# Kernel optimization log

Measured on AMD Instinct MI355X. Metric: run time of the kernel, lower is better.

Reference implementation:

```python
import jax, jax.numpy as jnp
import numpy as np

D_IN = 1024
D_OUT = 1024
NUM_HEADS = 16
HEAD_DIM = D_OUT // NUM_HEADS
ORDERS = 4


def setup_inputs() -> dict:
    key = jax.random.key(0)
    k_x, k_t, k_w, k_b, k_a = jax.random.split(key, 5)
    x = jax.random.normal(k_x, (8, 4096, D_IN), dtype=jnp.float32)
    t_scalar = jax.random.uniform(k_t, (), dtype=jnp.float32)
    # Linear params (torch nn.Linear: y = x @ W.T + b)
    W = jax.random.normal(k_w, (D_OUT, D_IN), dtype=jnp.float32) * (1.0 / np.sqrt(D_IN))
    b = jax.random.normal(k_b, (D_OUT,), dtype=jnp.float32) * 0.01
    A = jax.random.normal(k_a, (NUM_HEADS, HEAD_DIM, HEAD_DIM), dtype=jnp.float32) * 0.02
    return {"x": x, "t_scalar": t_scalar, "W": W, "b": b, "A": A}


def reference(x, t_scalar, W, b, A):
    # proj_in
    z = jnp.einsum('bsd,od->bso', x, W) + b  # [B, S, d_out]
    B, S, _ = z.shape
    z = z.reshape(B, S, NUM_HEADS, HEAD_DIM)
    # Taylor series: out = sum_{k=0}^{ORDERS} (t*A)^k z / k!
    out = z
    term = z
    for order in range(1, ORDERS + 1):
        term = jnp.einsum('hij,bnhj->bnhi', A, term) * (t_scalar / float(order))
        out = out + term
    return out.reshape(B, S, D_OUT)
```

## Files before the change

### kernel.cpp

```cpp
#include <hip/hip_runtime.h>
#include <hip/hip_bf16.h>
#include <cstdint>

#define NHEAD 16
#define ORDERS 4

typedef short short8 __attribute__((ext_vector_type(8)));
typedef float f32x4 __attribute__((ext_vector_type(4)));

__device__ __forceinline__ unsigned short f32_to_bf16_rtn(float f) {
  union { float f; unsigned u; } v; v.f = f;
  unsigned r = v.u + 0x7FFFu + ((v.u >> 16) & 1u);
  return (unsigned short)(r >> 16);
}

typedef __attribute__((address_space(1))) void gvoid;
typedef __attribute__((address_space(3))) void svoid;
__device__ __forceinline__ void gload_lds16(const void* g, void* l) {
  __builtin_amdgcn_global_load_lds((gvoid*)g, (svoid*)l, 16, 0, 0);
}

__global__ __launch_bounds__(256) void weff_kernel(
    const float* __restrict__ A, const float* __restrict__ t_ptr,
    const float* __restrict__ W, const float* __restrict__ bvec,
    unsigned short* __restrict__ Weff, float* __restrict__ beff) {
  __shared__ float Ah[64 * 65];
  __shared__ float T0[64 * 64];
  __shared__ float T1[64 * 64];

  const int tid = threadIdx.x;
  const int h = blockIdx.x >> 4;
  const int c = blockIdx.x & 15;
  const int d = tid & 63;
  const int ig = tid >> 6;

  float wreg[16];
  #pragma unroll
  for (int r = 0; r < 16; ++r)
    wreg[r] = W[(size_t)(h * 64 + ig * 16 + r) * 1024 + c * 64 + d];

  const float t = t_ptr[0];
  const int i = tid >> 2;
  const int jq = (tid & 3) << 4;

  for (int r = 0; r < 16; ++r) {
    int idx = tid + 256 * r;
    Ah[(idx >> 6) * 65 + (idx & 63)] = A[h * 4096 + idx];
  }
  float ms[16];
  #pragma unroll
  for (int cc = 0; cc < 16; ++cc) {
    float e = (i == jq + cc) ? 1.0f : 0.0f;
    T0[i * 64 + jq + cc] = e;
    ms[cc] = e;
  }
  __syncthreads();

  float* Tc = T0;
  float* Tn = T1;
  for (int k = 1; k <= ORDERS; ++k) {
    float scale = t / (float)k;
    float acc[16];
    #pragma unroll
    for (int cc = 0; cc < 16; ++cc) acc[cc] = 0.f;
    for (int l = 0; l < 64; ++l) {
      float a = Ah[i * 65 + l];
      float4 t0 = *(const float4*)&Tc[l * 64 + jq];
      float4 t1 = *(const float4*)&Tc[l * 64 + jq + 4];
      float4 t2 = *(const float4*)&Tc[l * 64 + jq + 8];
      float4 t3 = *(const float4*)&Tc[l * 64 + jq + 12];
      acc[0] += a * t0.x;  acc[1] += a * t0.y;  acc[2] += a * t0.z;  acc[3] += a * t0.w;
      acc[4] += a * t1.x;  acc[5] += a * t1.y;  acc[6] += a * t1.z;  acc[7] += a * t1.w;
      acc[8] += a * t2.x;  acc[9] += a * t2.y;  acc[10] += a * t2.z; acc[11] += a * t2.w;
      acc[12] += a * t3.x; acc[13] += a * t3.y; acc[14] += a * t3.z; acc[15] += a * t3.w;
    }
    #pragma unroll
    for (int cc = 0; cc < 16; ++cc) { acc[cc] *= scale; ms[cc] += acc[cc]; }
    #pragma unroll
    for (int u = 0; u < 4; ++u) {
      float4 v = {acc[u * 4], acc[u * 4 + 1], acc[u * 4 + 2], acc[u * 4 + 3]};
      *(float4*)&Tn[i * 64 + jq + u * 4] = v;
    }
    __syncthreads();
    float* tmp = Tc; Tc = Tn; Tn = tmp;
  }

  float* Mh = Ah;
  #pragma unroll
  for (int u = 0; u < 4; ++u) {
    float4 v = {ms[u * 4], ms[u * 4 + 1], ms[u * 4 + 2], ms[u * 4 + 3]};
    *(float4*)&Mh[i * 64 + jq + u * 4] = v;
  }
  float* Wc = T0;
  #pragma unroll
  for (int r = 0; r < 16; ++r) Wc[(ig * 16 + r) * 64 + d] = wreg[r];
  __syncthreads();

  #pragma unroll
  for (int ii = 0; ii < 16; ++ii) {
    int i2 = ig * 16 + ii;
    float acc = 0.f;
    #pragma unroll
    for (int j = 0; j < 64; ++j) acc += Mh[i2 * 64 + j] * Wc[j * 64 + d];
    Weff[(size_t)(h * 64 + i2) * 1024 + c * 64 + d] = f32_to_bf16_rtn(acc);
  }
  if (c == 0 && tid < 64) {
    float acc = 0.f;
    for (int j = 0; j < 64; ++j) acc += Mh[tid * 64 + j] * bvec[h * 64 + j];
    beff[h * 64 + tid] = acc;
  }
}

__global__ __launch_bounds__(256) void convert_x_kernel(
    const float* __restrict__ X, unsigned short* __restrict__ Xb, int n8) {
  int idx = blockIdx.x * blockDim.x + threadIdx.x;
  int stride = gridDim.x * blockDim.x;
  for (int i = idx; i < n8; i += stride) {
    float4 a = *(const float4*)(X + (size_t)i * 8);
    float4 b = *(const float4*)(X + (size_t)i * 8 + 4);
    unsigned short t[8] = {f32_to_bf16_rtn(a.x), f32_to_bf16_rtn(a.y),
                           f32_to_bf16_rtn(a.z), f32_to_bf16_rtn(a.w),
                           f32_to_bf16_rtn(b.x), f32_to_bf16_rtn(b.y),
                           f32_to_bf16_rtn(b.z), f32_to_bf16_rtn(b.w)};
    *(uint4*)(Xb + (size_t)i * 8) = *(const uint4*)t;
  }
}

#define CSTR 132

__global__ __launch_bounds__(256, 2) void gemm_kernel(
    const unsigned short* __restrict__ Xb, const unsigned short* __restrict__ Wf,
    const float* __restrict__ beff, float* __restrict__ Out) {
  __shared__ __align__(16) unsigned short smem[4 * 8192];

  const int wg = blockIdx.x;
  const int swz = (wg & 7) * 256 + (wg >> 3);
  const int by = swz >> 3;
  const int bx = swz & 7;
  const int R = by * 128;
  const int C = bx * 128;

  const int tid = threadIdx.x;
  const int lane = tid & 63;
  const int wave = tid >> 6;
  const int wm = wave >> 1;
  const int wn = wave & 1;
  const int frow = lane & 15;
  const int fkg = lane >> 4;

  f32x4 acc[4][4];
  #pragma unroll
  for (int mi = 0; mi < 4; ++mi)
    #pragma unroll
    for (int ni = 0; ni < 4; ++ni) acc[mi][ni] = (f32x4){0.f, 0.f, 0.f, 0.f};

  const int lr = lane >> 3;
  const int lc = lane & 7;
  const int scol = ((lc ^ lr) << 3);
  const unsigned short* Asrc = Xb + (size_t)(R + wave * 32 + lr) * 1024 + scol;
  const unsigned short* Bsrc = Wf + (size_t)(C + wave * 32 + lr) * 1024 + scol;

  auto stage = [&](int kt) {
    unsigned short* base = smem + (kt & 1) * 16384;
    char* Ad = (char*)(base + wave * 32 * 64);
    char* Bd = (char*)(base + 8192 + wave * 32 * 64);
    const int kb = kt * 64;
    #pragma unroll
    for (int i = 0; i < 4; ++i)
      gload_lds16(Asrc + (size_t)(i * 8) * 1024 + kb, Ad + i * 1024);
    #pragma unroll
    for (int i = 0; i < 4; ++i)
      gload_lds16(Bsrc + (size_t)(i * 8) * 1024 + kb, Bd + i * 1024);
  };

  stage(0);
  for (int kt = 0; kt < 16; ++kt) {
    if (kt < 15) {
      stage(kt + 1);
      asm volatile("s_waitcnt vmcnt(8)" ::: "memory");
    } else {
      asm volatile("s_waitcnt vmcnt(0)" ::: "memory");
    }
    __builtin_amdgcn_sched_barrier(0);
    __builtin_amdgcn_s_barrier();

    const unsigned short* As = smem + (kt & 1) * 16384;
    const unsigned short* Bs = As + 8192;
    short8 afr[4][2], bfr[4][2];
    #pragma unroll
    for (int mi = 0; mi < 4; ++mi) {
      int ar = wm * 64 + mi * 16 + frow;
      #pragma unroll
      for (int kk = 0; kk < 2; ++kk) {
        int slot = (kk * 4 + fkg) ^ (ar & 7);
        afr[mi][kk] = *(const short8*)&As[ar * 64 + slot * 8];
      }
    }
    #pragma unroll
    for (int ni = 0; ni < 4; ++ni) {
      int br = wn * 64 + ni * 16 + frow;
      #pragma unroll
      for (int kk = 0; kk < 2; ++kk) {
        int slot = (kk * 4 + fkg) ^ (br & 7);
        bfr[ni][kk] = *(const short8*)&Bs[br * 64 + slot * 8];
      }
    }
    asm volatile("s_waitcnt lgkmcnt(0)" ::: "memory");
    __builtin_amdgcn_sched_barrier(0);
    __builtin_amdgcn_s_barrier();

    #pragma unroll
    for (int mi = 0; mi < 4; ++mi)
      #pragma unroll
      for (int ni = 0; ni < 4; ++ni)
        #pragma unroll
        for (int kk = 0; kk < 2; ++kk)
          acc[mi][ni] = __builtin_amdgcn_mfma_f32_16x16x32_bf16(
              afr[mi][kk], bfr[ni][kk], acc[mi][ni], 0, 0, 0);
  }
  __syncthreads();

  float* Cs = (float*)smem;
  const int c4 = (tid & 31) << 2;
  float4 bb = *(const float4*)&beff[C + c4];
  #pragma unroll
  for (int mi = 0; mi < 4; ++mi) {
    #pragma unroll
    for (int ni = 0; ni < 4; ++ni) {
      int col = wn * 64 + ni * 16 + frow;
      #pragma unroll
      for (int reg = 0; reg < 4; ++reg)
        Cs[(wm * 16 + fkg * 4 + reg) * CSTR + col] = acc[mi][ni][reg];
    }
    __syncthreads();
    #pragma unroll
    for (int it = 0; it < 4; ++it) {
      int rloc = it * 8 + (tid >> 5);
      float4 v = *(const float4*)&Cs[rloc * CSTR + c4];
      v.x += bb.x; v.y += bb.y; v.z += bb.z; v.w += bb.w;
      int grow = R + (rloc >> 4) * 64 + mi * 16 + (rloc & 15);
      *(float4*)(Out + (size_t)grow * 1024 + C + c4) = v;
    }
    __syncthreads();
  }
}

#define LDSS 72
#define CSTRF 136
__global__ __launch_bounds__(256, 2) void gemm_fb(
    const float* __restrict__ X, const unsigned short* __restrict__ Weff,
    const float* __restrict__ beff, float* __restrict__ Out) {
  __shared__ __align__(16) unsigned short As0[128 * LDSS];
  __shared__ __align__(16) unsigned short As1[128 * LDSS];
  __shared__ __align__(16) unsigned short Bs0[128 * LDSS];
  __shared__ __align__(16) unsigned short Bs1[128 * LDSS];
  const int wg = blockIdx.x;
  const int swz = (wg & 7) * 256 + (wg >> 3);
  const int R = (swz >> 3) * 128;
  const int C = (swz & 7) * 128;
  const int tid = threadIdx.x;
  const int lane = tid & 63;
  const int wave = tid >> 6;
  const int wm = wave >> 1, wn = wave & 1;
  const int frow = lane & 15, fkg = lane >> 4;
  f32x4 acc[4][4];
  #pragma unroll
  for (int mi = 0; mi < 4; ++mi)
    #pragma unroll
    for (int ni = 0; ni < 4; ++ni) acc[mi][ni] = (f32x4){0.f, 0.f, 0.f, 0.f};
  const int ar = tid >> 4, akc = (tid & 15) << 2;
  const int bn_ = tid >> 3, bkc = (tid & 7) << 3;
  const float* Xbase = X + (size_t)(R + ar) * 1024 + akc;
  const unsigned short* Wbase = Weff + (size_t)(C + bn_) * 1024 + bkc;
  float4 av[8];
  uint4 bv[4];
  auto loadTile = [&](int kt) {
    const int kb = kt * 64;
    #pragma unroll
    for (int i = 0; i < 8; ++i) av[i] = *(const float4*)(Xbase + (size_t)i * 16 * 1024 + kb);
    #pragma unroll
    for (int i = 0; i < 4; ++i) bv[i] = *(const uint4*)(Wbase + (size_t)i * 32 * 1024 + kb);
  };
  auto writeTile = [&](unsigned short* Asn, unsigned short* Bsn) {
    #pragma unroll
    for (int i = 0; i < 8; ++i) {
      unsigned short tmp[4] = {f32_to_bf16_rtn(av[i].x), f32_to_bf16_rtn(av[i].y),
                               f32_to_bf16_rtn(av[i].z), f32_to_bf16_rtn(av[i].w)};
      *(uint2*)&Asn[(ar + i * 16) * LDSS + akc] = *(const uint2*)tmp;
    }
    #pragma unroll
    for (int i = 0; i < 4; ++i) *(uint4*)&Bsn[(bn_ + i * 32) * LDSS + bkc] = bv[i];
  };
  loadTile(0);
  writeTile(As0, Bs0);
  __syncthreads();
  unsigned short* Asc = As0; unsigned short* Asn = As1;
  unsigned short* Bsc = Bs0; unsigned short* Bsn = Bs1;
  for (int kt = 0; kt < 16; ++kt) {
    if (kt < 15) loadTile(kt + 1);
    short8 afr[4][2], bfr[4][2];
    #pragma unroll
    for (int mi = 0; mi < 4; ++mi)
      #pragma unroll
      for (int kk = 0; kk < 2; ++kk)
        afr[mi][kk] = *(const short8*)&Asc[(wm * 64 + mi * 16 + frow) * LDSS + kk * 32 + fkg * 8];
    #pragma unroll
    for (int ni = 0; ni < 4; ++ni)
      #pragma unroll
      for (int kk = 0; kk < 2; ++kk)
        bfr[ni][kk] = *(const short8*)&Bsc[(wn * 64 + ni * 16 + frow) * LDSS + kk * 32 + fkg * 8];
    #pragma unroll
    for (int mi = 0; mi < 4; ++mi)
      #pragma unroll
      for (int ni = 0; ni < 4; ++ni)
        #pragma unroll
        for (int kk = 0; kk < 2; ++kk)
          acc[mi][ni] = __builtin_amdgcn_mfma_f32_16x16x32_bf16(
              afr[mi][kk], bfr[ni][kk], acc[mi][ni], 0, 0, 0);
    if (kt < 15) writeTile(Asn, Bsn);
    __syncthreads();
    unsigned short* t1 = Asc; Asc = Asn; Asn = t1;
    unsigned short* t2 = Bsc; Bsc = Bsn; Bsn = t2;
  }
  float* Cs = (float*)As0;
  const int c4 = (tid & 31) << 2;
  float4 bb = *(const float4*)&beff[C + c4];
  #pragma unroll
  for (int mi = 0; mi < 4; ++mi) {
    #pragma unroll
    for (int ni = 0; ni < 4; ++ni) {
      int col = wn * 64 + ni * 16 + frow;
      #pragma unroll
      for (int reg = 0; reg < 4; ++reg)
        Cs[(wm * 16 + fkg * 4 + reg) * CSTRF + col] = acc[mi][ni][reg];
    }
    __syncthreads();
    #pragma unroll
    for (int it = 0; it < 4; ++it) {
      int rloc = it * 8 + (tid >> 5);
      float4 v = *(const float4*)&Cs[rloc * CSTRF + c4];
      v.x += bb.x; v.y += bb.y; v.z += bb.z; v.w += bb.w;
      int grow = R + (rloc >> 4) * 64 + mi * 16 + (rloc & 15);
      *(float4*)(Out + (size_t)grow * 1024 + C + c4) = v;
    }
    __syncthreads();
  }
}

extern "C" void kernel_launch(void* const* d_in, const int* in_sizes, int n_in,
                              void* d_out, int out_size, void* d_ws, size_t ws_size,
                              hipStream_t stream) {
  const float* x = (const float*)d_in[0];
  const float* t = (const float*)d_in[1];
  const float* W = (const float*)d_in[2];
  const float* b = (const float*)d_in[3];
  const float* A = (const float*)d_in[4];
  float* out = (float*)d_out;

  char* ws = (char*)d_ws;
  unsigned short* Weff = (unsigned short*)ws;
  float* beff = (float*)(ws + (2 << 20));
  unsigned short* Xb = (unsigned short*)(ws + (4ull << 20));

  const size_t need = (4ull << 20) + (64ull << 20);
  weff_kernel<<<256, 256, 0, stream>>>(A, t, W, b, Weff, beff);
  if (ws_size >= need) {
    convert_x_kernel<<<2048, 256, 0, stream>>>(x, Xb, 33554432 / 8);
    gemm_kernel<<<2048, 256, 0, stream>>>(Xb, Weff, beff, out);
  } else {
    gemm_fb<<<2048, 256, 0, stream>>>(x, Weff, beff, out);
  }
}
```

Baseline: 148.3 us.

## Switch bf16 GEMM to 256x256 tiles with phased 8-wave MFMA pipeline

Replaces the 128x128, 4-wave GEMM with a 256x256 tile computed by 8 waves, splitting each K step into four phases that interleave LDS fragment reads, async global-to-LDS staging, and MFMA blocks raised with s_setprio. The larger tile raises arithmetic intensity and cuts global and LDS traffic per output. The epilogue is rewritten to stage 64-row slabs through LDS with bias added. It uses 128KB of LDS per block and many more accumulator registers, which limits occupancy and leaves only 512 blocks.

Result: slower. 172.5 us (+16.3%).

```diff
diff --git a/kernel.cpp b/kernel.cpp
--- a/kernel.cpp
+++ b/kernel.cpp
@@ -126,120 +126,171 @@
   }
 }
 
-#define CSTR 132
-
-__global__ __launch_bounds__(256, 2) void gemm_kernel(
+#define MM16(MOFF, BSET, NOFF)                                                 \
+  {                                                                            \
+    _Pragma("unroll") for (int m_ = 0; m_ < 4; ++m_)                           \
+        _Pragma("unroll") for (int n_ = 0; n_ < 2; ++n_)                       \
+            _Pragma("unroll") for (int kk_ = 0; kk_ < 2; ++kk_)                \
+                acc[MOFF + m_][NOFF + n_] =                                    \
+        __builtin_amdgcn_mfma_f32_16x16x32_bf16(                               \
+            afr[m_][kk_], BSET[n_][kk_], acc[MOFF + m_][NOFF + n_], 0, 0, 0);  \
+  }
+
+__global__ __launch_bounds__(512, 2) void gemm256_kernel(
     const unsigned short* __restrict__ Xb, const unsigned short* __restrict__ Wf,
     const float* __restrict__ beff, float* __restrict__ Out) {
-  __shared__ __align__(16) unsigned short smem[4 * 8192];
+  __shared__ __align__(16) unsigned short smem[2 * 32768];
 
   const int wg = blockIdx.x;
-  const int swz = (wg & 7) * 256 + (wg >> 3);
-  const int by = swz >> 3;
-  const int bx = swz & 7;
-  const int R = by * 128;
-  const int C = bx * 128;
+  const int swz = (wg & 7) * 64 + (wg >> 3);
+  const int R = (swz >> 2) * 256;
+  const int C = (swz & 3) * 256;
 
   const int tid = threadIdx.x;
   const int lane = tid & 63;
-  const int wave = tid >> 6;
-  const int wm = wave >> 1;
-  const int wn = wave & 1;
+  const int w = tid >> 6;
+  const int wm = w >> 2;
+  const int wn = w & 3;
   const int frow = lane & 15;
   const int fkg = lane >> 4;
-
-  f32x4 acc[4][4];
-  #pragma unroll
-  for (int mi = 0; mi < 4; ++mi)
+  const int rx = frow & 7;
+
+  const int lr = lane >> 3;
+  const int scol = ((lane & 7) ^ lr) << 3;
+  const unsigned short* AsrcB = Xb + (size_t)(R + w * 8 + lr) * 1024 + scol;
+  const unsigned short* BsrcB = Wf + (size_t)(C + w * 8 + lr) * 1024 + scol;
+
+  auto stageB = [&](int j) {
+    char* bd = (char*)(smem + (j & 1) * 32768 + 16384) + w * 1024;
+    const unsigned short* s = BsrcB + j * 64;
+    #pragma unroll
+    for (int g = 0; g < 4; ++g)
+      gload_lds16(s + (size_t)(g * 64) * 1024, bd + g * 8192);
+  };
+  auto stageA = [&](int j, int half) {
+    char* ad = (char*)(smem + (j & 1) * 32768) + w * 1024;
+    const unsigned short* s = AsrcB + j * 64;
+    #pragma unroll
+    for (int g = 0; g < 2; ++g) {
+      int q = half + 2 * g;
+      gload_lds16(s + (size_t)(q * 64) * 1024, ad + q * 8192);
+    }
+  };
+
+  f32x4 acc[8][4];
+  #pragma unroll
+  for (int mi = 0; mi < 8; ++mi)
     #pragma unroll
     for (int ni = 0; ni < 4; ++ni) acc[mi][ni] = (f32x4){0.f, 0.f, 0.f, 0.f};
 
-  const int lr = lane >> 3;
-  const int lc = lane & 7;
-  const int scol = ((lc ^ lr) << 3);
-  const unsigned short* Asrc = Xb + (size_t)(R + wave * 32 + lr) * 1024 + scol;
-  const unsigned short* Bsrc = Wf + (size_t)(C + wave * 32 + lr) * 1024 + scol;
-
-  auto stage = [&](int kt) {
-    unsigned short* base = smem + (kt & 1) * 16384;
-    char* Ad = (char*)(base + wave * 32 * 64);
-    char* Bd = (char*)(base + 8192 + wave * 32 * 64);
-    const int kb = kt * 64;
-    #pragma unroll
-    for (int i = 0; i < 4; ++i)
-      gload_lds16(Asrc + (size_t)(i * 8) * 1024 + kb, Ad + i * 1024);
-    #pragma unroll
-    for (int i = 0; i < 4; ++i)
-      gload_lds16(Bsrc + (size_t)(i * 8) * 1024 + kb, Bd + i * 1024);
-  };
-
-  stage(0);
-  for (int kt = 0; kt < 16; ++kt) {
-    if (kt < 15) {
-      stage(kt + 1);
-      asm volatile("s_waitcnt vmcnt(8)" ::: "memory");
-    } else {
-      asm volatile("s_waitcnt vmcnt(0)" ::: "memory");
-    }
-    __builtin_amdgcn_sched_barrier(0);
-    __builtin_amdgcn_s_barrier();
-
-    const unsigned short* As = smem + (kt & 1) * 16384;
-    const unsigned short* Bs = As + 8192;
-    short8 afr[4][2], bfr[4][2];
-    #pragma unroll
-    for (int mi = 0; mi < 4; ++mi) {
-      int ar = wm * 64 + mi * 16 + frow;
-      #pragma unroll
-      for (int kk = 0; kk < 2; ++kk) {
-        int slot = (kk * 4 + fkg) ^ (ar & 7);
-        afr[mi][kk] = *(const short8*)&As[ar * 64 + slot * 8];
-      }
-    }
-    #pragma unroll
-    for (int ni = 0; ni < 4; ++ni) {
-      int br = wn * 64 + ni * 16 + frow;
-      #pragma unroll
-      for (int kk = 0; kk < 2; ++kk) {
-        int slot = (kk * 4 + fkg) ^ (br & 7);
-        bfr[ni][kk] = *(const short8*)&Bs[br * 64 + slot * 8];
-      }
-    }
+  short8 afr[4][2], b0[2][2], b1[2][2];
+  const int arow0 = wm * 128 + frow;
+  const int brow0 = wn * 64 + frow;
+  const int slot0 = (fkg ^ rx) << 3;
+  const int slot1 = ((4 + fkg) ^ rx) << 3;
+
+  auto rdA = [&](const unsigned short* buf, int msh) {
+    #pragma unroll
+    for (int m = 0; m < 4; ++m) {
+      int r = (arow0 + (msh * 4 + m) * 16) * 64;
+      afr[m][0] = *(const short8*)&buf[r + slot0];
+      afr[m][1] = *(const short8*)&buf[r + slot1];
+    }
+  };
+  auto rdB = [&](const unsigned short* buf, int nsh, short8 (&dst)[2][2]) {
+    #pragma unroll
+    for (int n = 0; n < 2; ++n) {
+      int r = 16384 + (brow0 + (nsh * 2 + n) * 16) * 64;
+      dst[n][0] = *(const short8*)&buf[r + slot0];
+      dst[n][1] = *(const short8*)&buf[r + slot1];
+    }
+  };
+
+  stageB(0);
+  stageA(0, 0);
+  stageA(0, 1);
+  stageA(1, 0);
+  stageA(1, 1);
+  asm volatile("s_waitcnt vmcnt(4)" ::: "memory");
+  __builtin_amdgcn_sched_barrier(0);
+  __builtin_amdgcn_s_barrier();
+
+  for (int j = 0; j < 16; ++j) {
+    const unsigned short* buf = smem + (j & 1) * 32768;
+
+    rdA(buf, 0);
+    rdB(buf, 0, b0);
+    if (j + 1 < 16) stageB(j + 1);
+    __builtin_amdgcn_s_barrier();
     asm volatile("s_waitcnt lgkmcnt(0)" ::: "memory");
     __builtin_amdgcn_sched_barrier(0);
-    __builtin_amdgcn_s_barrier();
-
-    #pragma unroll
-    for (int mi = 0; mi < 4; ++mi)
+    __builtin_amdgcn_s_setprio(1);
+    MM16(0, b0, 0);
+    __builtin_amdgcn_s_setprio(0);
+    __builtin_amdgcn_s_barrier();
+
+    rdB(buf, 1, b1);
+    if (j + 2 < 16) stageA(j + 2, 0);
+    __builtin_amdgcn_s_barrier();
+    asm volatile("s_waitcnt lgkmcnt(0)" ::: "memory");
+    __builtin_amdgcn_sched_barrier(0);
+    __builtin_amdgcn_s_setprio(1);
+    MM16(0, b1, 2);
+    __builtin_amdgcn_s_setprio(0);
+    __builtin_amdgcn_s_barrier();
+
+    rdA(buf, 1);
+    __builtin_amdgcn_s_barrier();
+    asm volatile("s_waitcnt lgkmcnt(0)" ::: "memory");
+    __builtin_amdgcn_sched_barrier(0);
+    __builtin_amdgcn_s_setprio(1);
+    MM16(4, b1, 2);
+    __builtin_amdgcn_s_setprio(0);
+    __builtin_amdgcn_s_barrier();
+
+    rdB(buf, 0, b0);
+    if (j + 2 < 16) stageA(j + 2, 1);
+    __builtin_amdgcn_s_barrier();
+    asm volatile("s_waitcnt lgkmcnt(0)" ::: "memory");
+    __builtin_amdgcn_sched_barrier(0);
+    __builtin_amdgcn_s_setprio(1);
+    MM16(4, b0, 0);
+    __builtin_amdgcn_s_setprio(0);
+    if (j <= 13) {
+      asm volatile("s_waitcnt vmcnt(4)" ::: "memory");
+    } else if (j == 14) {
+      asm volatile("s_waitcnt vmcnt(0)" ::: "memory");
+    }
+    __builtin_amdgcn_sched_barrier(0);
+    __builtin_amdgcn_s_barrier();
+  }
+  __syncthreads();
+
+  float* Cs = (float*)smem;
+  const int er = tid >> 3;
+  const int ecg = tid & 7;
+  float4 bias[8];
+  #pragma unroll
+  for (int u = 0; u < 8; ++u)
+    bias[u] = *(const float4*)&beff[C + ecg * 32 + u * 4];
+  #pragma unroll
+  for (int c = 0; c < 4; ++c) {
+    if (wm == (c >> 1)) {
       #pragma unroll
-      for (int ni = 0; ni < 4; ++ni)
+      for (int m = 0; m < 4; ++m)
         #pragma unroll
-        for (int kk = 0; kk < 2; ++kk)
-          acc[mi][ni] = __builtin_amdgcn_mfma_f32_16x16x32_bf16(
-              afr[mi][kk], bfr[ni][kk], acc[mi][ni], 0, 0, 0);
-  }
-  __syncthreads();
-
-  float* Cs = (float*)smem;
-  const int c4 = (tid & 31) << 2;
-  float4 bb = *(const float4*)&beff[C + c4];
-  #pragma unroll
-  for (int mi = 0; mi < 4; ++mi) {
-    #pragma unroll
-    for (int ni = 0; ni < 4; ++ni) {
-      int col = wn * 64 + ni * 16 + frow;
-      #pragma unroll
-      for (int reg = 0; reg < 4; ++reg)
-        Cs[(wm * 16 + fkg * 4 + reg) * CSTR + col] = acc[mi][ni][reg];
-    }
-    __syncthreads();
-    #pragma unroll
-    for (int it = 0; it < 4; ++it) {
-      int rloc = it * 8 + (tid >> 5);
-      float4 v = *(const float4*)&Cs[rloc * CSTR + c4];
-      v.x += bb.x; v.y += bb.y; v.z += bb.z; v.w += bb.w;
-      int grow = R + (rloc >> 4) * 64 + mi * 16 + (rloc & 15);
-      *(float4*)(Out + (size_t)grow * 1024 + C + c4) = v;
+        for (int ni = 0; ni < 4; ++ni)
+          #pragma unroll
+          for (int reg = 0; reg < 4; ++reg)
+            Cs[(m * 16 + fkg * 4 + reg) * 260 + wn * 64 + ni * 16 + frow] =
+                acc[(c & 1) * 4 + m][ni][reg];
+    }
+    __syncthreads();
+    #pragma unroll
+    for (int u = 0; u < 8; ++u) {
+      float4 v = *(const float4*)&Cs[er * 260 + ecg * 32 + u * 4];
+      v.x += bias[u].x; v.y += bias[u].y; v.z += bias[u].z; v.w += bias[u].w;
+      *(float4*)(Out + (size_t)(R + c * 64 + er) * 1024 + C + ecg * 32 + u * 4) = v;
     }
     __syncthreads();
   }
@@ -366,7 +417,7 @@
   weff_kernel<<<256, 256, 0, stream>>>(A, t, W, b, Weff, beff);
   if (ws_size >= need) {
     convert_x_kernel<<<2048, 256, 0, stream>>>(x, Xb, 33554432 / 8);
-    gemm_kernel<<<2048, 256, 0, stream>>>(Xb, Weff, beff, out);
+    gemm256_kernel<<<512, 512, 0, stream>>>(Xb, Weff, beff, out);
   } else {
     gemm_fb<<<2048, 256, 0, stream>>>(x, Weff, beff, out);
   }
```

## Enlarge GEMM tile to 256x256 with 8 waves and split LDS-read/MFMA phases

Applied to the files above, without the earlier changes.

Replaces the 128x128, 4-wave GEMM with a 256x256 tile using 512 threads and 128KB of double-buffered LDS. The larger tile halves global traffic per output. The main loop now splits A-fragment reads into two halves so the first MFMA batch can start while the second half of LDS reads is still in flight, and it drops one barrier and adds s_setprio around the MFMA blocks. In exchange, occupancy drops to one workgroup per CU, register pressure rises with 128 accumulator floats per thread, and the epilogue is reorganised into four 64-row store passes.

Result: slower. 175.6 us (+18.4%).

```diff
diff --git a/kernel.cpp b/kernel.cpp
--- a/kernel.cpp
+++ b/kernel.cpp
@@ -126,57 +126,54 @@
   }
 }
 
-#define CSTR 132
-
-__global__ __launch_bounds__(256, 2) void gemm_kernel(
+__global__ __launch_bounds__(512, 1) void gemm256_kernel(
     const unsigned short* __restrict__ Xb, const unsigned short* __restrict__ Wf,
     const float* __restrict__ beff, float* __restrict__ Out) {
-  __shared__ __align__(16) unsigned short smem[4 * 8192];
+  __shared__ __align__(16) char smem[131072];
 
   const int wg = blockIdx.x;
-  const int swz = (wg & 7) * 256 + (wg >> 3);
-  const int by = swz >> 3;
-  const int bx = swz & 7;
-  const int R = by * 128;
-  const int C = bx * 128;
+  const int swz = (wg & 7) * 64 + (wg >> 3);
+  const int R = (swz >> 2) * 256;
+  const int C = (swz & 3) * 256;
 
   const int tid = threadIdx.x;
   const int lane = tid & 63;
-  const int wave = tid >> 6;
-  const int wm = wave >> 1;
-  const int wn = wave & 1;
+  const int w = tid >> 6;
+  const int wm = w >> 2;
+  const int wn = w & 3;
   const int frow = lane & 15;
   const int fkg = lane >> 4;
-
-  f32x4 acc[4][4];
-  #pragma unroll
-  for (int mi = 0; mi < 4; ++mi)
+  const int fx = frow & 7;
+
+  f32x4 acc[8][4];
+  #pragma unroll
+  for (int mi = 0; mi < 8; ++mi)
     #pragma unroll
     for (int ni = 0; ni < 4; ++ni) acc[mi][ni] = (f32x4){0.f, 0.f, 0.f, 0.f};
 
-  const int lr = lane >> 3;
-  const int lc = lane & 7;
-  const int scol = ((lc ^ lr) << 3);
-  const unsigned short* Asrc = Xb + (size_t)(R + wave * 32 + lr) * 1024 + scol;
-  const unsigned short* Bsrc = Wf + (size_t)(C + wave * 32 + lr) * 1024 + scol;
+  const int lr8 = lane >> 3;
+  const int sl = lane & 7;
+  const int scol = ((sl ^ lr8) << 3);
+  const unsigned short* Asrc = Xb + (size_t)(R + w * 32 + lr8) * 1024 + scol;
+  const unsigned short* Bsrc = Wf + (size_t)(C + w * 32 + lr8) * 1024 + scol;
 
   auto stage = [&](int kt) {
-    unsigned short* base = smem + (kt & 1) * 16384;
-    char* Ad = (char*)(base + wave * 32 * 64);
-    char* Bd = (char*)(base + 8192 + wave * 32 * 64);
+    char* base = smem + (kt & 1) * 65536;
+    char* Ad = base + w * 4096;
+    char* Bd = base + 32768 + w * 4096;
     const int kb = kt * 64;
     #pragma unroll
-    for (int i = 0; i < 4; ++i)
-      gload_lds16(Asrc + (size_t)(i * 8) * 1024 + kb, Ad + i * 1024);
-    #pragma unroll
-    for (int i = 0; i < 4; ++i)
-      gload_lds16(Bsrc + (size_t)(i * 8) * 1024 + kb, Bd + i * 1024);
+    for (int u = 0; u < 4; ++u)
+      gload_lds16(Asrc + (size_t)(u * 8) * 1024 + kb, Ad + u * 1024);
+    #pragma unroll
+    for (int u = 0; u < 4; ++u)
+      gload_lds16(Bsrc + (size_t)(u * 8) * 1024 + kb, Bd + u * 1024);
   };
 
   stage(0);
-  for (int kt = 0; kt < 16; ++kt) {
-    if (kt < 15) {
-      stage(kt + 1);
+  for (int j = 0; j < 16; ++j) {
+    if (j < 15) {
+      stage(j + 1);
       asm volatile("s_waitcnt vmcnt(8)" ::: "memory");
     } else {
       asm volatile("s_waitcnt vmcnt(0)" ::: "memory");
@@ -184,31 +181,41 @@
     __builtin_amdgcn_sched_barrier(0);
     __builtin_amdgcn_s_barrier();
 
-    const unsigned short* As = smem + (kt & 1) * 16384;
-    const unsigned short* Bs = As + 8192;
-    short8 afr[4][2], bfr[4][2];
-    #pragma unroll
-    for (int mi = 0; mi < 4; ++mi) {
-      int ar = wm * 64 + mi * 16 + frow;
-      #pragma unroll
-      for (int kk = 0; kk < 2; ++kk) {
-        int slot = (kk * 4 + fkg) ^ (ar & 7);
-        afr[mi][kk] = *(const short8*)&As[ar * 64 + slot * 8];
-      }
-    }
+    const unsigned short* As = (const unsigned short*)(smem + (j & 1) * 65536);
+    const unsigned short* Bs = (const unsigned short*)(smem + (j & 1) * 65536 + 32768);
+
+    short8 bfr[4][2], afr0[4][2], afr1[4][2];
     #pragma unroll
     for (int ni = 0; ni < 4; ++ni) {
       int br = wn * 64 + ni * 16 + frow;
       #pragma unroll
       for (int kk = 0; kk < 2; ++kk) {
-        int slot = (kk * 4 + fkg) ^ (br & 7);
+        int slot = (kk * 4 + fkg) ^ fx;
         bfr[ni][kk] = *(const short8*)&Bs[br * 64 + slot * 8];
       }
     }
-    asm volatile("s_waitcnt lgkmcnt(0)" ::: "memory");
+    #pragma unroll
+    for (int mi = 0; mi < 4; ++mi) {
+      int ar = wm * 128 + mi * 16 + frow;
+      #pragma unroll
+      for (int kk = 0; kk < 2; ++kk) {
+        int slot = (kk * 4 + fkg) ^ fx;
+        afr0[mi][kk] = *(const short8*)&As[ar * 64 + slot * 8];
+      }
+    }
     __builtin_amdgcn_sched_barrier(0);
-    __builtin_amdgcn_s_barrier();
-
+    #pragma unroll
+    for (int mi = 0; mi < 4; ++mi) {
+      int ar = wm * 128 + 64 + mi * 16 + frow;
+      #pragma unroll
+      for (int kk = 0; kk < 2; ++kk) {
+        int slot = (kk * 4 + fkg) ^ fx;
+        afr1[mi][kk] = *(const short8*)&As[ar * 64 + slot * 8];
+      }
+    }
+    asm volatile("s_waitcnt lgkmcnt(8)" ::: "memory");
+    __builtin_amdgcn_sched_barrier(0);
+    __builtin_amdgcn_s_setprio(1);
     #pragma unroll
     for (int mi = 0; mi < 4; ++mi)
       #pragma unroll
@@ -216,30 +223,49 @@
         #pragma unroll
         for (int kk = 0; kk < 2; ++kk)
           acc[mi][ni] = __builtin_amdgcn_mfma_f32_16x16x32_bf16(
-              afr[mi][kk], bfr[ni][kk], acc[mi][ni], 0, 0, 0);
+              afr0[mi][kk], bfr[ni][kk], acc[mi][ni], 0, 0, 0);
+    __builtin_amdgcn_s_setprio(0);
+    asm volatile("s_waitcnt lgkmcnt(0)" ::: "memory");
+    __builtin_amdgcn_sched_barrier(0);
+    __builtin_amdgcn_s_setprio(1);
+    #pragma unroll
+    for (int mi = 0; mi < 4; ++mi)
+      #pragma unroll
+      for (int ni = 0; ni < 4; ++ni)
+        #pragma unroll
+        for (int kk = 0; kk < 2; ++kk)
+          acc[4 + mi][ni] = __builtin_amdgcn_mfma_f32_16x16x32_bf16(
+              afr1[mi][kk], bfr[ni][kk], acc[4 + mi][ni], 0, 0, 0);
+    __builtin_amdgcn_s_setprio(0);
+    __builtin_amdgcn_s_barrier();
   }
   __syncthreads();
 
   float* Cs = (float*)smem;
-  const int c4 = (tid & 31) << 2;
-  float4 bb = *(const float4*)&beff[C + c4];
-  #pragma unroll
-  for (int mi = 0; mi < 4; ++mi) {
-    #pragma unroll
-    for (int ni = 0; ni < 4; ++ni) {
-      int col = wn * 64 + ni * 16 + frow;
-      #pragma unroll
-      for (int reg = 0; reg < 4; ++reg)
-        Cs[(wm * 16 + fkg * 4 + reg) * CSTR + col] = acc[mi][ni][reg];
-    }
-    __syncthreads();
-    #pragma unroll
-    for (int it = 0; it < 4; ++it) {
-      int rloc = it * 8 + (tid >> 5);
-      float4 v = *(const float4*)&Cs[rloc * CSTR + c4];
-      v.x += bb.x; v.y += bb.y; v.z += bb.z; v.w += bb.w;
-      int grow = R + (rloc >> 4) * 64 + mi * 16 + (rloc & 15);
-      *(float4*)(Out + (size_t)grow * 1024 + C + c4) = v;
+  const int er = tid >> 3;
+  const int ecg = tid & 7;
+  float4 bias[8];
+  #pragma unroll
+  for (int u = 0; u < 8; ++u)
+    bias[u] = *(const float4*)&beff[C + ecg * 32 + u * 4];
+  #pragma unroll
+  for (int c = 0; c < 4; ++c) {
+    if (wm == (c >> 1)) {
+      #pragma unroll
+      for (int m = 0; m < 4; ++m)
+        #pragma unroll
+        for (int ni = 0; ni < 4; ++ni)
+          #pragma unroll
+          for (int reg = 0; reg < 4; ++reg)
+            Cs[(m * 16 + fkg * 4 + reg) * 260 + wn * 64 + ni * 16 + frow] =
+                acc[(c & 1) * 4 + m][ni][reg];
+    }
+    __syncthreads();
+    #pragma unroll
+    for (int u = 0; u < 8; ++u) {
+      float4 v = *(const float4*)&Cs[er * 260 + ecg * 32 + u * 4];
+      v.x += bias[u].x; v.y += bias[u].y; v.z += bias[u].z; v.w += bias[u].w;
+      *(float4*)(Out + (size_t)(R + c * 64 + er) * 1024 + C + ecg * 32 + u * 4) = v;
     }
     __syncthreads();
   }
@@ -366,7 +392,7 @@
   weff_kernel<<<256, 256, 0, stream>>>(A, t, W, b, Weff, beff);
   if (ws_size >= need) {
     convert_x_kernel<<<2048, 256, 0, stream>>>(x, Xb, 33554432 / 8);
-    gemm_kernel<<<2048, 256, 0, stream>>>(Xb, Weff, beff, out);
+    gemm256_kernel<<<512, 512, 0, stream>>>(Xb, Weff, beff, out);
   } else {
     gemm_fb<<<2048, 256, 0, stream>>>(x, Weff, beff, out);
   }
```

## Single-buffer B tile to cut LDS and raise GEMM occupancy to three blocks

Applied to the files above, without the earlier changes.

The B tile in LDS becomes a single buffer, refilled right after fragments are read into registers, while A stays double-buffered. This cuts shared memory from 64KB to 48KB per block so launch bounds can target three blocks per CU, hiding more memory latency. It also raises wave priority around the MFMA block. The risks are that B loads now sit less far ahead of their use, and that fewer registers per thread at the higher occupancy target could cause spills.

Result: faster. 139.6 us, median of 2 (-5.9%).

```diff
diff --git a/kernel.cpp b/kernel.cpp
--- a/kernel.cpp
+++ b/kernel.cpp
@@ -128,17 +128,15 @@
 
 #define CSTR 132
 
-__global__ __launch_bounds__(256, 2) void gemm_kernel(
+__global__ __launch_bounds__(256, 3) void gemm_kernel(
     const unsigned short* __restrict__ Xb, const unsigned short* __restrict__ Wf,
     const float* __restrict__ beff, float* __restrict__ Out) {
-  __shared__ __align__(16) unsigned short smem[4 * 8192];
+  __shared__ __align__(16) char smem[49152];
 
   const int wg = blockIdx.x;
   const int swz = (wg & 7) * 256 + (wg >> 3);
-  const int by = swz >> 3;
-  const int bx = swz & 7;
-  const int R = by * 128;
-  const int C = bx * 128;
+  const int R = (swz >> 3) * 128;
+  const int C = (swz & 7) * 128;
 
   const int tid = threadIdx.x;
   const int lane = tid & 63;
@@ -154,38 +152,41 @@
     #pragma unroll
     for (int ni = 0; ni < 4; ++ni) acc[mi][ni] = (f32x4){0.f, 0.f, 0.f, 0.f};
 
-  const int lr = lane >> 3;
+  const int lr8 = lane >> 3;
   const int lc = lane & 7;
-  const int scol = ((lc ^ lr) << 3);
-  const unsigned short* Asrc = Xb + (size_t)(R + wave * 32 + lr) * 1024 + scol;
-  const unsigned short* Bsrc = Wf + (size_t)(C + wave * 32 + lr) * 1024 + scol;
-
-  auto stage = [&](int kt) {
-    unsigned short* base = smem + (kt & 1) * 16384;
-    char* Ad = (char*)(base + wave * 32 * 64);
-    char* Bd = (char*)(base + 8192 + wave * 32 * 64);
+  const int scol = ((lc ^ lr8) << 3);
+  const unsigned short* Asrc = Xb + (size_t)(R + wave * 32 + lr8) * 1024 + scol;
+  const unsigned short* Bsrc = Wf + (size_t)(C + wave * 32 + lr8) * 1024 + scol;
+
+  auto stageA = [&](int kt, int bufSel) {
+    char* Ad = smem + bufSel * 16384 + wave * 4096;
     const int kb = kt * 64;
     #pragma unroll
     for (int i = 0; i < 4; ++i)
       gload_lds16(Asrc + (size_t)(i * 8) * 1024 + kb, Ad + i * 1024);
+  };
+  auto stageB = [&](int kt) {
+    char* Bd = smem + 32768 + wave * 4096;
+    const int kb = kt * 64;
     #pragma unroll
     for (int i = 0; i < 4; ++i)
       gload_lds16(Bsrc + (size_t)(i * 8) * 1024 + kb, Bd + i * 1024);
   };
 
-  stage(0);
+  stageA(0, 0);
+  stageB(0);
   for (int kt = 0; kt < 16; ++kt) {
     if (kt < 15) {
-      stage(kt + 1);
-      asm volatile("s_waitcnt vmcnt(8)" ::: "memory");
+      stageA(kt + 1, (kt + 1) & 1);
+      asm volatile("s_waitcnt vmcnt(4)" ::: "memory");
     } else {
       asm volatile("s_waitcnt vmcnt(0)" ::: "memory");
     }
     __builtin_amdgcn_sched_barrier(0);
     __builtin_amdgcn_s_barrier();
 
-    const unsigned short* As = smem + (kt & 1) * 16384;
-    const unsigned short* Bs = As + 8192;
+    const unsigned short* As = (const unsigned short*)(smem + (kt & 1) * 16384);
+    const unsigned short* Bb = (const unsigned short*)(smem + 32768);
     short8 afr[4][2], bfr[4][2];
     #pragma unroll
     for (int mi = 0; mi < 4; ++mi) {
@@ -202,13 +203,16 @@
       #pragma unroll
       for (int kk = 0; kk < 2; ++kk) {
         int slot = (kk * 4 + fkg) ^ (br & 7);
-        bfr[ni][kk] = *(const short8*)&Bs[br * 64 + slot * 8];
+        bfr[ni][kk] = *(const short8*)&Bb[br * 64 + slot * 8];
       }
     }
     asm volatile("s_waitcnt lgkmcnt(0)" ::: "memory");
     __builtin_amdgcn_sched_barrier(0);
     __builtin_amdgcn_s_barrier();
 
+    if (kt < 15) stageB(kt + 1);
+
+    __builtin_amdgcn_s_setprio(1);
     #pragma unroll
     for (int mi = 0; mi < 4; ++mi)
       #pragma unroll
@@ -217,6 +221,7 @@
         for (int kk = 0; kk < 2; ++kk)
           acc[mi][ni] = __builtin_amdgcn_mfma_f32_16x16x32_bf16(
               afr[mi][kk], bfr[ni][kk], acc[mi][ni], 0, 0, 0);
+    __builtin_amdgcn_s_setprio(0);
   }
   __syncthreads();
 
```
